# Kernel optimization log

Hardware: AMD Instinct MI355X
Metric: run time of the kernel (lower is better)

The kernel has to match this reference:

```python
import jax, jax.numpy as jnp
import numpy as np

N = 50000      # nodes
E = 800000     # edges (avg degree 16)
IN = 128       # in_dim == hidden_dim*num_heads so residuals fire
D = 32         # hidden_dim (per-head)
H = 4          # num_heads
OUT = 64       # out_dim (final layer has 1 head)
NEG_SLOPE = 0.2
LN_EPS = 1e-5


def setup_inputs() -> dict:
    key = jax.random.key(0)
    ks = jax.random.split(key, 16)
    rn = lambda k, s: jax.random.normal(k, s, jnp.float32) * 0.05
    return {
        "features": jax.random.normal(ks[0], (N, IN), jnp.float32),
        "edge_weight": jax.random.uniform(ks[1], (E,), jnp.float32),
        "src": jax.random.randint(ks[2], (E,), 0, N),
        "dst": jax.random.randint(ks[3], (E,), 0, N),
        "W0": rn(ks[4], (IN, H * D)), "al0": rn(ks[5], (H, D)), "ar0": rn(ks[6], (H, D)), "lam0": jnp.float32(1.0),
        "W1": rn(ks[7], (H * D, H * D)), "al1": rn(ks[8], (H, D)), "ar1": rn(ks[9], (H, D)), "lam1": jnp.float32(1.0),
        "W2": rn(ks[10], (H * D, OUT)), "al2": rn(ks[11], (1, OUT)), "ar2": rn(ks[12], (1, OUT)), "lam2": jnp.float32(1.0),
        "g0": jnp.ones((H * D,), jnp.float32), "b0": jnp.zeros((H * D,), jnp.float32),
        "g1": jnp.ones((H * D,), jnp.float32), "b1": jnp.zeros((H * D,), jnp.float32),
    }


def _gat_layer(h, W, al, ar, lam, src, dst, ew):
    n = h.shape[0]
    heads, d = al.shape
    ft = (h @ W).reshape(n, heads, d)                      # [N,H,D]
    el = jnp.sum(ft * al[None], axis=-1)                   # [N,H]
    er = jnp.sum(ft * ar[None], axis=-1)                   # [N,H]
    e = el[src] + er[dst] + lam * ew[:, None]              # [E,H] u_add_v + weight bias
    e = jax.nn.leaky_relu(e, NEG_SLOPE)
    # edge softmax over incoming edges of each dst node
    m = jax.ops.segment_max(e, dst, num_segments=n)        # [N,H]
    ex = jnp.exp(e - m[dst])
    s = jax.ops.segment_sum(ex, dst, num_segments=n)       # [N,H]
    a = ex / s[dst]                                        # [E,H]
    # u_mul_e + sum aggregation
    msg = ft[src] * a[:, :, None]                          # [E,H,D]
    return jax.ops.segment_sum(msg, dst, num_segments=n)   # [N,H,D]


def _layer_norm(x, g, b):
    mu = jnp.mean(x, axis=-1, keepdims=True)
    var = jnp.mean((x - mu) ** 2, axis=-1, keepdims=True)
    return (x - mu) * jax.lax.rsqrt(var + LN_EPS) * g + b


def _forward(features, edge_weight, src, dst,
             W0, al0, ar0, lam0, W1, al1, ar1, lam1, W2, al2, ar2, lam2,
             g0, b0, g1, b1):
    n = features.shape[0]
    h = features
    # layer 0
    h1 = _gat_layer(h, W0, al0, ar0, lam0, src, dst, edge_weight)
    h1 = jax.nn.elu(h1).reshape(n, -1)
    h1 = _layer_norm(h1, g0, b0)
    if h1.shape == h.shape:
        h1 = h1 + h
    # layer 1
    h2 = _gat_layer(h1, W1, al1, ar1, lam1, src, dst, edge_weight)
    h2 = jax.nn.elu(h2).reshape(n, -1)
    h2 = _layer_norm(h2, g1, b1)
    h2 = h2 + h1
    # layer 2 (single head, no activation)
    out = _gat_layer(h2, W2, al2, ar2, lam2, src, dst, edge_weight).reshape(n, -1)
    return out


def reference(features, edge_weight, src, dst,
              W0, al0, ar0, lam0, W1, al1, ar1, lam1, W2, al2, ar2, lam2,
              g0, b0, g1, b1):
    # eval mode: dropout off and _add_noise is identity, so noisy == clean
    h_clean = _forward(features, edge_weight, src, dst,
                       W0, al0, ar0, lam0, W1, al1, ar1, lam1, W2, al2, ar2, lam2,
                       g0, b0, g1, b1)
    return (h_clean, h_clean)
```

## Files before the change

kernel.cpp:

```cpp
#include <hip/hip_runtime.h>

#define NEG_SLOPE 0.2f
#define LN_EPS 1e-5f

typedef __attribute__((ext_vector_type(8))) short bf16x8;
typedef __attribute__((ext_vector_type(4))) float f32x4;

__device__ inline unsigned short f2bf(float f) {
    unsigned u = __float_as_uint(f);
    unsigned r = u + 0x7FFFu + ((u >> 16) & 1u);
    return (unsigned short)(r >> 16);
}

__device__ inline void unpack8(uint4 u, float* f) {
    f[0] = __uint_as_float(u.x << 16);
    f[1] = __uint_as_float(u.x & 0xFFFF0000u);
    f[2] = __uint_as_float(u.y << 16);
    f[3] = __uint_as_float(u.y & 0xFFFF0000u);
    f[4] = __uint_as_float(u.z << 16);
    f[5] = __uint_as_float(u.z & 0xFFFF0000u);
    f[6] = __uint_as_float(u.w << 16);
    f[7] = __uint_as_float(u.w & 0xFFFF0000u);
}


__global__ void rank_kernel(const int* __restrict__ dst, int* __restrict__ counts,
                            int* __restrict__ rank, int E) {
    int i = blockIdx.x * blockDim.x + threadIdx.x;
    if (i < E) rank[i] = atomicAdd(&counts[dst[i] * 16], 1);
}

__global__ __launch_bounds__(256) void scan1_kernel(const int* __restrict__ counts,
                                                    int* __restrict__ bsum, int n) {
    __shared__ int lds[256];
    int t = threadIdx.x;
    int i = blockIdx.x * 256 + t;
    lds[t] = (i < n) ? counts[i * 16] : 0;
    __syncthreads();
    for (int off = 128; off > 0; off >>= 1) {
        int v = (t < off) ? lds[t + off] : 0;
        __syncthreads();
        if (t < off) lds[t] += v;
        __syncthreads();
    }
    if (t == 0) bsum[blockIdx.x] = lds[0];
}

__global__ __launch_bounds__(256) void scan2_kernel(int* __restrict__ bsum, int nblocks) {
    __shared__ int lds[256];
    int t = threadIdx.x;
    int v0 = (t < nblocks) ? bsum[t] : 0;
    lds[t] = v0;
    __syncthreads();
    for (int off = 1; off < 256; off <<= 1) {
        int v = (t >= off) ? lds[t - off] : 0;
        __syncthreads();
        lds[t] += v;
        __syncthreads();
    }
    if (t < nblocks) bsum[t] = lds[t] - v0;
}

__global__ __launch_bounds__(256) void scan3_kernel(const int* __restrict__ counts,
                                                    const int* __restrict__ bsum,
                                                    int* __restrict__ rowptr, int n, int E) {
    __shared__ int lds[256];
    int t = threadIdx.x;
    int i = blockIdx.x * 256 + t;
    int c = (i < n) ? counts[i * 16] : 0;
    lds[t] = c;
    __syncthreads();
    for (int off = 1; off < 256; off <<= 1) {
        int v = (t >= off) ? lds[t - off] : 0;
        __syncthreads();
        lds[t] += v;
        __syncthreads();
    }
    if (i < n) rowptr[i] = bsum[blockIdx.x] + lds[t] - c;
    if (i == n) rowptr[n] = E;
}

__global__ void place_kernel(const int* __restrict__ src, const int* __restrict__ dst,
                             const float* __restrict__ ew, const int* __restrict__ rowptr,
                             const int* __restrict__ rank, unsigned* __restrict__ edge_p,
                             int E) {
    int i = blockIdx.x * blockDim.x + threadIdx.x;
    if (i < E) {
        int p = rowptr[dst[i]] + rank[i];
        edge_p[p] = ((unsigned)f2bf(ew[i]) << 16) | (unsigned)src[i];
    }
}


__global__ void fcast_kernel(const float4* __restrict__ in, uint2* __restrict__ out, int n4) {
    int i = blockIdx.x * blockDim.x + threadIdx.x;
    if (i < n4) {
        float4 v = in[i];
        out[i] = make_uint2((unsigned)f2bf(v.x) | ((unsigned)f2bf(v.y) << 16),
                            (unsigned)f2bf(v.z) | ((unsigned)f2bf(v.w) << 16));
    }
}

__global__ void wcast_all(const float* __restrict__ W0, const float* __restrict__ W1,
                          const float* __restrict__ W2, unsigned short* __restrict__ Wt0,
                          unsigned short* __restrict__ Wt1, unsigned short* __restrict__ Wt2) {
    int bn = blockIdx.x, k = threadIdx.x;
    if (bn < 128) {
        Wt0[bn * 128 + k] = f2bf(W0[k * 128 + bn]);
    } else if (bn < 256) {
        int c = bn - 128;
        Wt1[c * 128 + k] = f2bf(W1[k * 128 + c]);
    } else {
        int c = bn - 256;
        Wt2[c * 128 + k] = f2bf(W2[k * 64 + c]);
    }
}


template <int NT, int H>
__global__ __launch_bounds__(256) void gemm_mfma(const uint4* __restrict__ A,
                                                 const unsigned short* __restrict__ Wt,
                                                 const float* __restrict__ al,
                                                 const float* __restrict__ ar,
                                                 unsigned short* __restrict__ ftb,
                                                 float* __restrict__ el,
                                                 float* __restrict__ er, int n) {
    constexpr int LDA = 136;
    constexpr int D = NT * 16 / H;
    __shared__ unsigned short As[64 * LDA];
    __shared__ unsigned short Ws[NT * 16 * LDA];
    int t = threadIdx.x;
    int row0 = blockIdx.x * 64;

    #pragma unroll
    for (int j = 0; j < 4; ++j) {
        int idx = t + j * 256;
        int r = idx >> 4;
        int c8 = idx & 15;
        int row = row0 + r;
        uint4 v = (row < n) ? A[(size_t)row * 16 + c8] : make_uint4(0, 0, 0, 0);
        *(uint4*)&As[r * LDA + c8 * 8] = v;
    }
    const uint4* Wg = (const uint4*)Wt;
    #pragma unroll
    for (int j = 0; j < NT; ++j) {
        int idx = t + j * 256;
        int r = idx >> 4;
        int c8 = idx & 15;
        *(uint4*)&Ws[r * LDA + c8 * 8] = Wg[idx];
    }
    __syncthreads();

    int w = t >> 6, lane = t & 63;
    int m = lane & 15, q = lane >> 4;
    f32x4 acc[NT] = {};
    const unsigned short* ap = &As[(w * 16 + m) * LDA + q * 8];
    #pragma unroll
    for (int kk = 0; kk < 4; ++kk) {
        bf16x8 a = *(const bf16x8*)(ap + kk * 32);
        #pragma unroll
        for (int nt = 0; nt < NT; ++nt) {
            bf16x8 b = *(const bf16x8*)&Ws[(nt * 16 + m) * LDA + kk * 32 + q * 8];
            acc[nt] = __builtin_amdgcn_mfma_f32_16x16x32_bf16(a, b, acc[nt], 0, 0, 0);
        }
    }

    float alv[NT], arv[NT];
    #pragma unroll
    for (int nt = 0; nt < NT; ++nt) {
        alv[nt] = al[nt * 16 + m];
        arv[nt] = ar[nt * 16 + m];
    }

    int orow = row0 + w * 16 + q * 4;
    #pragma unroll
    for (int r = 0; r < 4; ++r) {
        int row = orow + r;
        float pl[H] = {}, pr[H] = {};
        #pragma unroll
        for (int nt = 0; nt < NT; ++nt) {
            int h = (nt * 16) / D;
            pl[h] = fmaf(acc[nt][r], alv[nt], pl[h]);
            pr[h] = fmaf(acc[nt][r], arv[nt], pr[h]);
        }
        #pragma unroll
        for (int off = 1; off < 16; off <<= 1) {
            #pragma unroll
            for (int h = 0; h < H; ++h) {
                pl[h] += __shfl_xor(pl[h], off, 64);
                pr[h] += __shfl_xor(pr[h], off, 64);
            }
        }
        if (row < n) {
            #pragma unroll
            for (int nt = 0; nt < NT; ++nt)
                ftb[(size_t)row * (NT * 16) + nt * 16 + m] = f2bf(acc[nt][r]);
            if (m < H) {
                float vl = pl[0], vr = pr[0];
                #pragma unroll
                for (int h = 1; h < H; ++h)
                    if (m == h) { vl = pl[h]; vr = pr[h]; }
                el[row * H + m] = vl;
                er[row * H + m] = vr;
            }
        }
    }
}


__device__ inline void accum8(float* ax, uint4 u, float p) {
    ax[0] = fmaf(p, __uint_as_float(u.x << 16), ax[0]);
    ax[1] = fmaf(p, __uint_as_float(u.x & 0xFFFF0000u), ax[1]);
    ax[2] = fmaf(p, __uint_as_float(u.y << 16), ax[2]);
    ax[3] = fmaf(p, __uint_as_float(u.y & 0xFFFF0000u), ax[3]);
    ax[4] = fmaf(p, __uint_as_float(u.z << 16), ax[4]);
    ax[5] = fmaf(p, __uint_as_float(u.z & 0xFFFF0000u), ax[5]);
    ax[6] = fmaf(p, __uint_as_float(u.w << 16), ax[6]);
    ax[7] = fmaf(p, __uint_as_float(u.w & 0xFFFF0000u), ax[7]);
}

__global__ __launch_bounds__(256) void gat_agg_ln(
    const int* __restrict__ rowptr, const unsigned* __restrict__ edge_p,
    const uint4* __restrict__ ftb4, const float* __restrict__ el,
    const float* __restrict__ er, const float* __restrict__ lam_p,
    const float* __restrict__ g, const float* __restrict__ b,
    const uint4* __restrict__ prevb, uint4* __restrict__ outb, int n) {
    int node = blockIdx.x * 16 + (threadIdx.x >> 4);
    if (node >= n) return;
    int li = threadIdx.x & 15;
    int head = li >> 2;
    float lam = lam_p[0];
    float erv = er[node * 4 + head];
    int s0 = rowptr[node], s1 = rowptr[node + 1];
    float ax[8] = {};
    float s = 0.f;

    int i = s0;
    for (; i + 4 <= s1; i += 4) {
        unsigned e0 = edge_p[i], e1 = edge_p[i + 1], e2 = edge_p[i + 2], e3 = edge_p[i + 3];
        unsigned sn0 = e0 & 0xFFFFu, sn1 = e1 & 0xFFFFu, sn2 = e2 & 0xFFFFu, sn3 = e3 & 0xFFFFu;
        uint4 u0 = ftb4[(size_t)sn0 * 16 + li];
        uint4 u1 = ftb4[(size_t)sn1 * 16 + li];
        uint4 u2 = ftb4[(size_t)sn2 * 16 + li];
        uint4 u3 = ftb4[(size_t)sn3 * 16 + li];
        float l0 = el[sn0 * 4 + head];
        float l1 = el[sn1 * 4 + head];
        float l2 = el[sn2 * 4 + head];
        float l3 = el[sn3 * 4 + head];
        float v0 = l0 + erv + lam * __uint_as_float(e0 & 0xFFFF0000u);
        float v1 = l1 + erv + lam * __uint_as_float(e1 & 0xFFFF0000u);
        float v2 = l2 + erv + lam * __uint_as_float(e2 & 0xFFFF0000u);
        float v3 = l3 + erv + lam * __uint_as_float(e3 & 0xFFFF0000u);
        v0 = fmaxf(v0, NEG_SLOPE * v0);
        v1 = fmaxf(v1, NEG_SLOPE * v1);
        v2 = fmaxf(v2, NEG_SLOPE * v2);
        v3 = fmaxf(v3, NEG_SLOPE * v3);
        float p0 = __expf(v0), p1 = __expf(v1), p2 = __expf(v2), p3 = __expf(v3);
        accum8(ax, u0, p0);
        accum8(ax, u1, p1);
        accum8(ax, u2, p2);
        accum8(ax, u3, p3);
        s += (p0 + p1) + (p2 + p3);
    }
    for (; i < s1; ++i) {
        unsigned e = edge_p[i];
        unsigned sn = e & 0xFFFFu;
        uint4 u = ftb4[(size_t)sn * 16 + li];
        float v = el[sn * 4 + head] + erv + lam * __uint_as_float(e & 0xFFFF0000u);
        v = fmaxf(v, NEG_SLOPE * v);
        float p = __expf(v);
        accum8(ax, u, p);
        s += p;
    }

    float inv = (s > 0.f) ? 1.f / s : 0.f;
    float x[8];
    float sum = 0.f, sq = 0.f;
    #pragma unroll
    for (int d = 0; d < 8; ++d) {
        float v = ax[d] * inv;
        v = (v > 0.f) ? v : expm1f(v);
        x[d] = v;
        sum += v;
        sq += v * v;
    }
    #pragma unroll
    for (int off = 1; off < 16; off <<= 1) {
        sum += __shfl_xor(sum, off, 16);
        sq += __shfl_xor(sq, off, 16);
    }
    float mu = sum * (1.f / 128.f);
    float var = sq * (1.f / 128.f) - mu * mu;
    float rs = rsqrtf(var + LN_EPS);

    const float4* g4 = (const float4*)g;
    const float4* b4 = (const float4*)b;
    float pv[8];
    unpack8(prevb[(size_t)node * 16 + li], pv);
    float y[8];
    #pragma unroll
    for (int h = 0; h < 2; ++h) {
        float4 gv = g4[li * 2 + h];
        float4 bv = b4[li * 2 + h];
        y[h * 4 + 0] = (x[h * 4 + 0] - mu) * rs * gv.x + bv.x + pv[h * 4 + 0];
        y[h * 4 + 1] = (x[h * 4 + 1] - mu) * rs * gv.y + bv.y + pv[h * 4 + 1];
        y[h * 4 + 2] = (x[h * 4 + 2] - mu) * rs * gv.z + bv.z + pv[h * 4 + 2];
        y[h * 4 + 3] = (x[h * 4 + 3] - mu) * rs * gv.w + bv.w + pv[h * 4 + 3];
    }
    uint4 o;
    o.x = (unsigned)f2bf(y[0]) | ((unsigned)f2bf(y[1]) << 16);
    o.y = (unsigned)f2bf(y[2]) | ((unsigned)f2bf(y[3]) << 16);
    o.z = (unsigned)f2bf(y[4]) | ((unsigned)f2bf(y[5]) << 16);
    o.w = (unsigned)f2bf(y[6]) | ((unsigned)f2bf(y[7]) << 16);
    outb[(size_t)node * 16 + li] = o;
}

__global__ __launch_bounds__(256) void gat_agg_out(
    const int* __restrict__ rowptr, const unsigned* __restrict__ edge_p,
    const uint2* __restrict__ ftb2, const float* __restrict__ el,
    const float* __restrict__ er, const float* __restrict__ lam_p,
    float* __restrict__ out, int n) {
    int node = blockIdx.x * 16 + (threadIdx.x >> 4);
    if (node >= n) return;
    int li = threadIdx.x & 15;
    float lam = lam_p[0];
    float erv = er[node];
    int s0 = rowptr[node], s1 = rowptr[node + 1];
    float ax[4] = {};
    float s = 0.f;

    int i = s0;
    for (; i + 4 <= s1; i += 4) {
        unsigned e0 = edge_p[i], e1 = edge_p[i + 1], e2 = edge_p[i + 2], e3 = edge_p[i + 3];
        unsigned sn0 = e0 & 0xFFFFu, sn1 = e1 & 0xFFFFu, sn2 = e2 & 0xFFFFu, sn3 = e3 & 0xFFFFu;
        uint2 u0 = ftb2[(size_t)sn0 * 16 + li];
        uint2 u1 = ftb2[(size_t)sn1 * 16 + li];
        uint2 u2 = ftb2[(size_t)sn2 * 16 + li];
        uint2 u3 = ftb2[(size_t)sn3 * 16 + li];
        float l0 = el[sn0], l1 = el[sn1], l2 = el[sn2], l3 = el[sn3];
        float v0 = l0 + erv + lam * __uint_as_float(e0 & 0xFFFF0000u);
        float v1 = l1 + erv + lam * __uint_as_float(e1 & 0xFFFF0000u);
        float v2 = l2 + erv + lam * __uint_as_float(e2 & 0xFFFF0000u);
        float v3 = l3 + erv + lam * __uint_as_float(e3 & 0xFFFF0000u);
        v0 = fmaxf(v0, NEG_SLOPE * v0);
        v1 = fmaxf(v1, NEG_SLOPE * v1);
        v2 = fmaxf(v2, NEG_SLOPE * v2);
        v3 = fmaxf(v3, NEG_SLOPE * v3);
        float p0 = __expf(v0), p1 = __expf(v1), p2 = __expf(v2), p3 = __expf(v3);
        ax[0] = fmaf(p0, __uint_as_float(u0.x << 16), ax[0]);
        ax[1] = fmaf(p0, __uint_as_float(u0.x & 0xFFFF0000u), ax[1]);
        ax[2] = fmaf(p0, __uint_as_float(u0.y << 16), ax[2]);
        ax[3] = fmaf(p0, __uint_as_float(u0.y & 0xFFFF0000u), ax[3]);
        ax[0] = fmaf(p1, __uint_as_float(u1.x << 16), ax[0]);
        ax[1] = fmaf(p1, __uint_as_float(u1.x & 0xFFFF0000u), ax[1]);
        ax[2] = fmaf(p1, __uint_as_float(u1.y << 16), ax[2]);
        ax[3] = fmaf(p1, __uint_as_float(u1.y & 0xFFFF0000u), ax[3]);
        ax[0] = fmaf(p2, __uint_as_float(u2.x << 16), ax[0]);
        ax[1] = fmaf(p2, __uint_as_float(u2.x & 0xFFFF0000u), ax[1]);
        ax[2] = fmaf(p2, __uint_as_float(u2.y << 16), ax[2]);
        ax[3] = fmaf(p2, __uint_as_float(u2.y & 0xFFFF0000u), ax[3]);
        ax[0] = fmaf(p3, __uint_as_float(u3.x << 16), ax[0]);
        ax[1] = fmaf(p3, __uint_as_float(u3.x & 0xFFFF0000u), ax[1]);
        ax[2] = fmaf(p3, __uint_as_float(u3.y << 16), ax[2]);
        ax[3] = fmaf(p3, __uint_as_float(u3.y & 0xFFFF0000u), ax[3]);
        s += (p0 + p1) + (p2 + p3);
    }
    for (; i < s1; ++i) {
        unsigned e = edge_p[i];
        unsigned sn = e & 0xFFFFu;
        uint2 u = ftb2[(size_t)sn * 16 + li];
        float v = el[sn] + erv + lam * __uint_as_float(e & 0xFFFF0000u);
        v = fmaxf(v, NEG_SLOPE * v);
        float p = __expf(v);
        ax[0] = fmaf(p, __uint_as_float(u.x << 16), ax[0]);
        ax[1] = fmaf(p, __uint_as_float(u.x & 0xFFFF0000u), ax[1]);
        ax[2] = fmaf(p, __uint_as_float(u.y << 16), ax[2]);
        ax[3] = fmaf(p, __uint_as_float(u.y & 0xFFFF0000u), ax[3]);
        s += p;
    }

    float inv = (s > 0.f) ? 1.f / s : 0.f;
    float4 y;
    y.x = ax[0] * inv;
    y.y = ax[1] * inv;
    y.z = ax[2] * inv;
    y.w = ax[3] * inv;
    ((float4*)out)[(size_t)node * 16 + li] = y;
    ((float4*)out)[(size_t)(n + node) * 16 + li] = y;
}


extern "C" void kernel_launch(void* const* d_in, const int* in_sizes, int n_in,
                              void* d_out, int out_size, void* d_ws, size_t ws_size,
                              hipStream_t stream) {
    const float* features = (const float*)d_in[0];
    const float* edge_weight = (const float*)d_in[1];
    const int* src = (const int*)d_in[2];
    const int* dst = (const int*)d_in[3];
    const float* W0 = (const float*)d_in[4];
    const float* al0 = (const float*)d_in[5];
    const float* ar0 = (const float*)d_in[6];
    const float* lam0 = (const float*)d_in[7];
    const float* W1 = (const float*)d_in[8];
    const float* al1 = (const float*)d_in[9];
    const float* ar1 = (const float*)d_in[10];
    const float* lam1 = (const float*)d_in[11];
    const float* W2 = (const float*)d_in[12];
    const float* al2 = (const float*)d_in[13];
    const float* ar2 = (const float*)d_in[14];
    const float* lam2 = (const float*)d_in[15];
    const float* g0 = (const float*)d_in[16];
    const float* b0 = (const float*)d_in[17];
    const float* g1 = (const float*)d_in[18];
    const float* b1 = (const float*)d_in[19];

    const int N = in_sizes[0] / 128;
    const int E = in_sizes[1];

    char* w = (char*)d_ws;
    size_t o = 0;
    auto carve = [&](size_t bytes) {
        char* p = w + o;
        o += (bytes + 255) & ~(size_t)255;
        return p;
    };
    int* counts = (int*)carve((size_t)N * 64);
    int* rowptr = (int*)carve((size_t)(N + 1) * 4);
    int* bsum = (int*)carve(256 * 4);
    int* rank = (int*)carve((size_t)E * 4);
    unsigned* edge_p = (unsigned*)carve((size_t)E * 4);
    unsigned short* ftb = (unsigned short*)carve((size_t)N * 128 * 2);
    unsigned short* f0b = (unsigned short*)carve((size_t)N * 128 * 2);
    unsigned short* h1 = (unsigned short*)carve((size_t)N * 128 * 2);
    unsigned short* h2 = (unsigned short*)carve((size_t)N * 128 * 2);
    float* el = (float*)carve((size_t)N * 4 * 4);
    float* er = (float*)carve((size_t)N * 4 * 4);
    unsigned short* Wt0 = (unsigned short*)carve(128 * 128 * 2);
    unsigned short* Wt1 = (unsigned short*)carve(128 * 128 * 2);
    unsigned short* Wt2 = (unsigned short*)carve(64 * 128 * 2);

    const int nscan = (N + 255) / 256;
    const int ngemm = (N + 63) / 64;
    const int nagg = (N + 15) / 16;

    hipMemsetAsync(counts, 0, (size_t)N * 64, stream);
    rank_kernel<<<(E + 255) / 256, 256, 0, stream>>>(dst, counts, rank, E);
    scan1_kernel<<<nscan, 256, 0, stream>>>(counts, bsum, N);
    scan2_kernel<<<1, 256, 0, stream>>>(bsum, nscan);
    scan3_kernel<<<(N + 1 + 255) / 256, 256, 0, stream>>>(counts, bsum, rowptr, N, E);
    place_kernel<<<(E + 255) / 256, 256, 0, stream>>>(src, dst, edge_weight, rowptr,
                                                      rank, edge_p, E);
    fcast_kernel<<<(N * 32 + 255) / 256, 256, 0, stream>>>((const float4*)features,
                                                           (uint2*)f0b, N * 32);
    wcast_all<<<320, 128, 0, stream>>>(W0, W1, W2, Wt0, Wt1, Wt2);

    gemm_mfma<8, 4><<<ngemm, 256, 0, stream>>>((const uint4*)f0b, Wt0, al0, ar0,
                                               ftb, el, er, N);
    gat_agg_ln<<<nagg, 256, 0, stream>>>(rowptr, edge_p, (const uint4*)ftb, el, er, lam0,
                                         g0, b0, (const uint4*)f0b, (uint4*)h1, N);
    gemm_mfma<8, 4><<<ngemm, 256, 0, stream>>>((const uint4*)h1, Wt1, al1, ar1,
                                               ftb, el, er, N);
    gat_agg_ln<<<nagg, 256, 0, stream>>>(rowptr, edge_p, (const uint4*)ftb, el, er, lam1,
                                         g1, b1, (const uint4*)h1, (uint4*)h2, N);
    gemm_mfma<4, 1><<<ngemm, 256, 0, stream>>>((const uint4*)h2, Wt2, al2, ar2,
                                               ftb, el, er, N);
    gat_agg_out<<<nagg, 256, 0, stream>>>(rowptr, edge_p, (const uint2*)ftb,
                                          el, er, lam2, (float*)d_out, N);
}
```

Measured before the change: 307.9 us.

## Fuse input cast into first GEMM, merge prep kernels and scan stages

Removes the separate feature fp32-to-bf16 cast kernel: the first GEMM now loads fp32 features and converts while staging into LDS, and the first aggregation reads the fp32 residual directly. The weight transpose-cast is folded into the rank/atomic kernel as extra blocks, and the single-block scan2 is merged into scan3, where every block redundantly scans the block sums. This cuts three kernel launches and one full N×128 intermediate write and read, in exchange for more fp32 traffic in the first GEMM and residual read.

```diff
diff --git a/kernel.cpp b/kernel.cpp
--- a/kernel.cpp
+++ b/kernel.cpp
@@ -24,10 +24,29 @@
 }
 
 
-__global__ void rank_kernel(const int* __restrict__ dst, int* __restrict__ counts,
-                            int* __restrict__ rank, int E) {
-    int i = blockIdx.x * blockDim.x + threadIdx.x;
-    if (i < E) rank[i] = atomicAdd(&counts[dst[i] * 16], 1);
+__global__ void prep_kernel(const int* __restrict__ dst, int* __restrict__ counts,
+                            int* __restrict__ rank, int E, int RB,
+                            const float* __restrict__ W0, const float* __restrict__ W1,
+                            const float* __restrict__ W2, unsigned short* __restrict__ Wt0,
+                            unsigned short* __restrict__ Wt1,
+                            unsigned short* __restrict__ Wt2) {
+    int bid = blockIdx.x;
+    if (bid < RB) {
+        int i = bid * 256 + threadIdx.x;
+        if (i < E) rank[i] = atomicAdd(&counts[dst[i] * 16], 1);
+    } else {
+        int row = (bid - RB) * 2 + (threadIdx.x >> 7);
+        int k = threadIdx.x & 127;
+        if (row < 128) {
+            Wt0[row * 128 + k] = f2bf(W0[k * 128 + row]);
+        } else if (row < 256) {
+            int c = row - 128;
+            Wt1[c * 128 + k] = f2bf(W1[k * 128 + c]);
+        } else {
+            int c = row - 256;
+            Wt2[c * 128 + k] = f2bf(W2[k * 64 + c]);
+        }
+    }
 }
 
 __global__ __launch_bounds__(256) void scan1_kernel(const int* __restrict__ counts,
@@ -46,11 +65,13 @@
     if (t == 0) bsum[blockIdx.x] = lds[0];
 }
 
-__global__ __launch_bounds__(256) void scan2_kernel(int* __restrict__ bsum, int nblocks) {
+__global__ __launch_bounds__(256) void scan3_kernel(const int* __restrict__ counts,
+                                                    const int* __restrict__ bsum,
+                                                    int* __restrict__ rowptr, int n, int E,
+                                                    int nscan) {
     __shared__ int lds[256];
     int t = threadIdx.x;
-    int v0 = (t < nblocks) ? bsum[t] : 0;
-    lds[t] = v0;
+    lds[t] = (t < nscan) ? bsum[t] : 0;
     __syncthreads();
     for (int off = 1; off < 256; off <<= 1) {
         int v = (t >= off) ? lds[t - off] : 0;
@@ -58,14 +79,8 @@
         lds[t] += v;
         __syncthreads();
     }
-    if (t < nblocks) bsum[t] = lds[t] - v0;
-}
-
-__global__ __launch_bounds__(256) void scan3_kernel(const int* __restrict__ counts,
-                                                    const int* __restrict__ bsum,
-                                                    int* __restrict__ rowptr, int n, int E) {
-    __shared__ int lds[256];
-    int t = threadIdx.x;
+    int boff = (blockIdx.x > 0) ? lds[blockIdx.x - 1] : 0;
+    __syncthreads();
     int i = blockIdx.x * 256 + t;
     int c = (i < n) ? counts[i * 16] : 0;
     lds[t] = c;
@@ -76,7 +91,7 @@
         lds[t] += v;
         __syncthreads();
     }
-    if (i < n) rowptr[i] = bsum[blockIdx.x] + lds[t] - c;
+    if (i < n) rowptr[i] = boff + lds[t] - c;
     if (i == n) rowptr[n] = E;
 }
 
@@ -92,33 +107,8 @@
 }
 
 
-__global__ void fcast_kernel(const float4* __restrict__ in, uint2* __restrict__ out, int n4) {
-    int i = blockIdx.x * blockDim.x + threadIdx.x;
-    if (i < n4) {
-        float4 v = in[i];
-        out[i] = make_uint2((unsigned)f2bf(v.x) | ((unsigned)f2bf(v.y) << 16),
-                            (unsigned)f2bf(v.z) | ((unsigned)f2bf(v.w) << 16));
-    }
-}
-
-__global__ void wcast_all(const float* __restrict__ W0, const float* __restrict__ W1,
-                          const float* __restrict__ W2, unsigned short* __restrict__ Wt0,
-                          unsigned short* __restrict__ Wt1, unsigned short* __restrict__ Wt2) {
-    int bn = blockIdx.x, k = threadIdx.x;
-    if (bn < 128) {
-        Wt0[bn * 128 + k] = f2bf(W0[k * 128 + bn]);
-    } else if (bn < 256) {
-        int c = bn - 128;
-        Wt1[c * 128 + k] = f2bf(W1[k * 128 + c]);
-    } else {
-        int c = bn - 256;
-        Wt2[c * 128 + k] = f2bf(W2[k * 64 + c]);
-    }
-}
-
-
-template <int NT, int H>
-__global__ __launch_bounds__(256) void gemm_mfma(const uint4* __restrict__ A,
+template <int NT, int H, bool A32>
+__global__ __launch_bounds__(256) void gemm_mfma(const void* __restrict__ Ap,
                                                  const unsigned short* __restrict__ Wt,
                                                  const float* __restrict__ al,
                                                  const float* __restrict__ ar,
@@ -132,14 +122,30 @@
     int t = threadIdx.x;
     int row0 = blockIdx.x * 64;
 
-    #pragma unroll
-    for (int j = 0; j < 4; ++j) {
-        int idx = t + j * 256;
-        int r = idx >> 4;
-        int c8 = idx & 15;
-        int row = row0 + r;
-        uint4 v = (row < n) ? A[(size_t)row * 16 + c8] : make_uint4(0, 0, 0, 0);
-        *(uint4*)&As[r * LDA + c8 * 8] = v;
+    if constexpr (A32) {
+        const float4* A4 = (const float4*)Ap;
+        #pragma unroll
+        for (int j = 0; j < 8; ++j) {
+            int idx = t + j * 256;
+            int r = idx >> 5;
+            int c4 = idx & 31;
+            int row = row0 + r;
+            float4 v = (row < n) ? A4[(size_t)row * 32 + c4] : make_float4(0.f, 0.f, 0.f, 0.f);
+            unsigned p0 = (unsigned)f2bf(v.x) | ((unsigned)f2bf(v.y) << 16);
+            unsigned p1 = (unsigned)f2bf(v.z) | ((unsigned)f2bf(v.w) << 16);
+            *(uint2*)&As[r * LDA + c4 * 4] = make_uint2(p0, p1);
+        }
+    } else {
+        const uint4* A16 = (const uint4*)Ap;
+        #pragma unroll
+        for (int j = 0; j < 4; ++j) {
+            int idx = t + j * 256;
+            int r = idx >> 4;
+            int c8 = idx & 15;
+            int row = row0 + r;
+            uint4 v = (row < n) ? A16[(size_t)row * 16 + c8] : make_uint4(0, 0, 0, 0);
+            *(uint4*)&As[r * LDA + c8 * 8] = v;
+        }
     }
     const uint4* Wg = (const uint4*)Wt;
     #pragma unroll
@@ -219,12 +225,13 @@
     ax[7] = fmaf(p, __uint_as_float(u.w & 0xFFFF0000u), ax[7]);
 }
 
+template <bool PREV32>
 __global__ __launch_bounds__(256) void gat_agg_ln(
     const int* __restrict__ rowptr, const unsigned* __restrict__ edge_p,
     const uint4* __restrict__ ftb4, const float* __restrict__ el,
     const float* __restrict__ er, const float* __restrict__ lam_p,
     const float* __restrict__ g, const float* __restrict__ b,
-    const uint4* __restrict__ prevb, uint4* __restrict__ outb, int n) {
+    const void* __restrict__ prevp, uint4* __restrict__ outb, int n) {
     int node = blockIdx.x * 16 + (threadIdx.x >> 4);
     if (node >= n) return;
     int li = threadIdx.x & 15;
@@ -296,7 +303,17 @@
     const float4* g4 = (const float4*)g;
     const float4* b4 = (const float4*)b;
     float pv[8];
-    unpack8(prevb[(size_t)node * 16 + li], pv);
+    if constexpr (PREV32) {
+        const float4* p4 = (const float4*)prevp;
+        #pragma unroll
+        for (int h = 0; h < 2; ++h) {
+            float4 v = p4[(size_t)node * 32 + li * 2 + h];
+            pv[h * 4 + 0] = v.x; pv[h * 4 + 1] = v.y;
+            pv[h * 4 + 2] = v.z; pv[h * 4 + 3] = v.w;
+        }
+    } else {
+        unpack8(((const uint4*)prevp)[(size_t)node * 16 + li], pv);
+    }
     float y[8];
     #pragma unroll
     for (int h = 0; h < 2; ++h) {
@@ -430,7 +447,6 @@
     int* rank = (int*)carve((size_t)E * 4);
     unsigned* edge_p = (unsigned*)carve((size_t)E * 4);
     unsigned short* ftb = (unsigned short*)carve((size_t)N * 128 * 2);
-    unsigned short* f0b = (unsigned short*)carve((size_t)N * 128 * 2);
     unsigned short* h1 = (unsigned short*)carve((size_t)N * 128 * 2);
     unsigned short* h2 = (unsigned short*)carve((size_t)N * 128 * 2);
     float* el = (float*)carve((size_t)N * 4 * 4);
@@ -442,28 +458,24 @@
     const int nscan = (N + 255) / 256;
     const int ngemm = (N + 63) / 64;
     const int nagg = (N + 15) / 16;
+    const int RB = (E + 255) / 256;
 
     hipMemsetAsync(counts, 0, (size_t)N * 64, stream);
-    rank_kernel<<<(E + 255) / 256, 256, 0, stream>>>(dst, counts, rank, E);
+    prep_kernel<<<RB + 160, 256, 0, stream>>>(dst, counts, rank, E, RB,
+                                              W0, W1, W2, Wt0, Wt1, Wt2);
     scan1_kernel<<<nscan, 256, 0, stream>>>(counts, bsum, N);
-    scan2_kernel<<<1, 256, 0, stream>>>(bsum, nscan);
-    scan3_kernel<<<(N + 1 + 255) / 256, 256, 0, stream>>>(counts, bsum, rowptr, N, E);
+    scan3_kernel<<<(N + 1 + 255) / 256, 256, 0, stream>>>(counts, bsum, rowptr, N, E, nscan);
     place_kernel<<<(E + 255) / 256, 256, 0, stream>>>(src, dst, edge_weight, rowptr,
                                                       rank, edge_p, E);
-    fcast_kernel<<<(N * 32 + 255) / 256, 256, 0, stream>>>((const float4*)features,
-                                                           (uint2*)f0b, N * 32);
-    wcast_all<<<320, 128, 0, stream>>>(W0, W1, W2, Wt0, Wt1, Wt2);
-
-    gemm_mfma<8, 4><<<ngemm, 256, 0, stream>>>((const uint4*)f0b, Wt0, al0, ar0,
-                                               ftb, el, er, N);
-    gat_agg_ln<<<nagg, 256, 0, stream>>>(rowptr, edge_p, (const uint4*)ftb, el, er, lam0,
-                                         g0, b0, (const uint4*)f0b, (uint4*)h1, N);
-    gemm_mfma<8, 4><<<ngemm, 256, 0, stream>>>((const uint4*)h1, Wt1, al1, ar1,
-                                               ftb, el, er, N);
-    gat_agg_ln<<<nagg, 256, 0, stream>>>(rowptr, edge_p, (const uint4*)ftb, el, er, lam1,
-                                         g1, b1, (const uint4*)h1, (uint4*)h2, N);
-    gemm_mfma<4, 1><<<ngemm, 256, 0, stream>>>((const uint4*)h2, Wt2, al2, ar2,
-                                               ftb, el, er, N);
+
+    gemm_mfma<8, 4, true><<<ngemm, 256, 0, stream>>>(features, Wt0, al0, ar0,
+                                                     ftb, el, er, N);
+    gat_agg_ln<true><<<nagg, 256, 0, stream>>>(rowptr, edge_p, (const uint4*)ftb, el, er,
+                                               lam0, g0, b0, features, (uint4*)h1, N);
+    gemm_mfma<8, 4, false><<<ngemm, 256, 0, stream>>>(h1, Wt1, al1, ar1, ftb, el, er, N);
+    gat_agg_ln<false><<<nagg, 256, 0, stream>>>(rowptr, edge_p, (const uint4*)ftb, el, er,
+                                                lam1, g1, b1, h1, (uint4*)h2, N);
+    gemm_mfma<4, 1, false><<<ngemm, 256, 0, stream>>>(h2, Wt2, al2, ar2, ftb, el, er, N);
     gat_agg_out<<<nagg, 256, 0, stream>>>(rowptr, edge_p, (const uint2*)ftb,
                                           el, er, lam2, (float*)d_out, N);
 }
```

After: 295.3 us. 4.1% less time.
